# Optimization experiments

Measured on AMD Instinct MI355X. Metric: run time of the kernel, lower is better.

Reference implementation:

```python
import jax, jax.numpy as jnp
import numpy as np
import math

B, N, H, NH, HD, G = 2, 1024, 512, 8, 64, 50
MAX_DIST = 10.0


def setup_inputs() -> dict:
    key = jax.random.key(0)
    ks = jax.random.split(key, 12)
    s = 0.02  # small init scale for weights
    return {
        'x': jax.random.normal(ks[0], (B, N, H), jnp.float32),
        'distances': jax.random.uniform(ks[1], (B, N, N), jnp.float32) * MAX_DIST,
        'mask': jnp.ones((B, N), jnp.int32),
        'widths': jnp.ones((G,), jnp.float32) * 0.5,
        'dp_w': jax.random.normal(ks[2], (G, NH), jnp.float32) * s,
        'dp_b': jnp.zeros((NH,), jnp.float32),
        'wq': jax.random.normal(ks[3], (H, H), jnp.float32) * s,
        'bq': jnp.zeros((H,), jnp.float32),
        'wk': jax.random.normal(ks[4], (H, H), jnp.float32) * s,
        'bk': jnp.zeros((H,), jnp.float32),
        'wv': jax.random.normal(ks[5], (H, H), jnp.float32) * s,
        'bv': jnp.zeros((H,), jnp.float32),
        'wo': jax.random.normal(ks[6], (H, H), jnp.float32) * s,
        'bo': jnp.zeros((H,), jnp.float32),
        'ln1_g': jnp.ones((H,), jnp.float32),
        'ln1_b': jnp.zeros((H,), jnp.float32),
        'ln2_g': jnp.ones((H,), jnp.float32),
        'ln2_b': jnp.zeros((H,), jnp.float32),
        'w1': jax.random.normal(ks[7], (H, 4 * H), jnp.float32) * s,
        'b1': jnp.zeros((4 * H,), jnp.float32),
        'w2': jax.random.normal(ks[8], (4 * H, H), jnp.float32) * s,
        'b2': jnp.zeros((H,), jnp.float32),
    }


def _layernorm(x, g, b, eps=1e-5):
    mu = jnp.mean(x, axis=-1, keepdims=True)
    var = jnp.mean(jnp.square(x - mu), axis=-1, keepdims=True)
    return (x - mu) * jax.lax.rsqrt(var + eps) * g + b


def reference(x, distances, mask, widths, dp_w, dp_b, wq, bq, wk, bk, wv, bv,
              wo, bo, ln1_g, ln1_b, ln2_g, ln2_b, w1, b1, w2, b2):
    centers = jnp.linspace(0.0, MAX_DIST, G, dtype=jnp.float32)  # buffer

    residual = x
    xn = _layernorm(x, ln1_g, ln1_b)

    def split_heads(t):  # [B,N,H] -> [B,NH,N,HD]
        return t.reshape(B, N, NH, HD).transpose(0, 2, 1, 3)

    q = split_heads(xn @ wq + bq)
    k = split_heads(xn @ wk + bk)
    v = split_heads(xn @ wv + bv)

    scores = jnp.einsum('bhqd,bhkd->bhqk', q, k) / math.sqrt(HD)

    # Gaussian distance encoding: [B,N,N,G]
    diff = distances[..., None] - centers
    gf = jnp.exp(-jnp.square(diff) / (2.0 * jnp.square(widths)))
    # project to per-head bias, then permute to [B,NH,N,N]
    dist_bias = (gf @ dp_w + dp_b).transpose(0, 3, 1, 2)
    scores = scores + dist_bias

    key_mask = mask[:, None, None, :]  # [B,1,1,N]
    scores = jnp.where(key_mask == 0, -1e9, scores)

    attn = jax.nn.softmax(scores, axis=-1)
    out = jnp.einsum('bhqk,bhkd->bhqd', attn, v)
    out = out.transpose(0, 2, 1, 3).reshape(B, N, H)
    out = out @ wo + bo

    x = residual + out
    residual = x
    xn = _layernorm(x, ln2_g, ln2_b)
    h = jax.nn.gelu(xn @ w1 + b1, approximate=False)  # dropout is identity in eval
    x = residual + (h @ w2 + b2)
    return x
```

## Files before the change

kernel.cpp:

```cpp
#include <hip/hip_runtime.h>
#include <hip/hip_bf16.h>
#include <math.h>

#define B_ 2
#define N_ 1024
#define H_ 512
#define NH_ 8
#define HD_ 64
#define G_ 50
#define TAB_ 1024
constexpr float MAXD = 10.0f;

typedef __attribute__((ext_vector_type(8))) short short8;
typedef __attribute__((ext_vector_type(4))) float f32x4;

__device__ inline ushort f2bf(float v) {
  __hip_bfloat16 h = __float2bfloat16(v);
  return *(ushort*)&h;
}
__device__ inline float bf2f(ushort u) {
  unsigned x = ((unsigned)u) << 16;
  return __uint_as_float(x);
}
__device__ inline void gload_lds16(const ushort* g, ushort* l) {
  __builtin_amdgcn_global_load_lds(
      (const __attribute__((address_space(1))) void*)g,
      (__attribute__((address_space(3))) void*)l, 16, 0, 0);
}

__device__ inline void transp_dev(const float* __restrict__ src,
                                  ushort* __restrict__ d, int R, int C,
                                  int bx, int by, int t, float (*tile)[33]) {
  int r0 = by * 32, c0 = bx * 32;
  int rr = t >> 5, cc = t & 31;
  #pragma unroll
  for (int p = 0; p < 4; ++p)
    tile[rr + p * 8][cc] = src[(size_t)(r0 + rr + p * 8) * C + c0 + cc];
  __syncthreads();
  #pragma unroll
  for (int p = 0; p < 4; ++p)
    d[(size_t)(c0 + rr + p * 8) * R + r0 + cc] = f2bf(tile[cc][rr + p * 8]);
}

__global__ __launch_bounds__(256) void prep_k(
    const float* wq, const float* wk, const float* wv, const float* wo,
    const float* w1, const float* w2, ushort* __restrict__ wT4,
    ushort* __restrict__ w1T, ushort* __restrict__ w2T,
    const float* __restrict__ widths, const float* __restrict__ dp_w,
    const float* __restrict__ dp_b, float2* __restrict__ tab2,
    const float* __restrict__ x, const float* __restrict__ ln1g,
    const float* __restrict__ ln1b, ushort* __restrict__ xn) {
  __shared__ float tile[32][33];
  __shared__ float red2[4][2];
  int bid = blockIdx.x, t = threadIdx.x;
  if (bid < 1024) {
    int z = bid >> 8, rem = bid & 255;
    const float* src = (z == 0) ? wq : (z == 1) ? wk : (z == 2) ? wv : wo;
    transp_dev(src, wT4 + (size_t)z * 512 * 512, 512, 512, rem & 15, rem >> 4, t, tile);
  } else if (bid < 2048) {
    int rem = bid - 1024;
    transp_dev(w1, w1T, 512, 2048, rem & 63, rem >> 6, t, tile);
  } else if (bid < 3072) {
    int rem = bid - 2048;
    transp_dev(w2, w2T, 2048, 512, rem & 15, rem >> 4, t, tile);
  } else if (bid < 3105) {
    int i = (bid - 3072) * 256 + t;
    if (i >= NH_ * (TAB_ + 1)) return;
    int h = i / (TAB_ + 1), tt = i % (TAB_ + 1);
    int t1 = tt < TAB_ ? tt + 1 : tt;
    float d0 = (float)tt * (MAXD / TAB_);
    float d1 = (float)t1 * (MAXD / TAB_);
    float v0 = dp_b[h], v1 = dp_b[h];
    for (int g = 0; g < G_; ++g) {
      float c = (float)g * (MAXD / 49.0f);
      float w = widths[g];
      float inv = -1.0f / (2.0f * w * w);
      float wg = dp_w[g * NH_ + h];
      float e0 = d0 - c, e1 = d1 - c;
      v0 += expf(e0 * e0 * inv) * wg;
      v1 += expf(e1 * e1 * inv) * wg;
    }
    tab2[i] = make_float2(v0, v1);
  } else {
    int row = (bid - 3105) * 2 + (t >> 7);
    int tl = t & 127;
    float4 v = *(const float4*)(x + (size_t)row * H_ + tl * 4);
    float s = v.x + v.y + v.z + v.w;
    float sq = v.x * v.x + v.y * v.y + v.z * v.z + v.w * v.w;
    #pragma unroll
    for (int m = 1; m < 64; m <<= 1) {
      s += __shfl_xor(s, m, 64);
      sq += __shfl_xor(sq, m, 64);
    }
    int wid = t >> 6;
    if ((t & 63) == 0) { red2[wid][0] = s; red2[wid][1] = sq; }
    __syncthreads();
    int rw = (t >> 7) * 2;
    s = red2[rw][0] + red2[rw + 1][0];
    sq = red2[rw][1] + red2[rw + 1][1];
    float mu = s * (1.0f / H_);
    float var = sq * (1.0f / H_) - mu * mu;
    float rs = rsqrtf(var + 1e-5f);
    float4 gg = *(const float4*)(ln1g + tl * 4);
    float4 bb = *(const float4*)(ln1b + tl * 4);
    ushort4 o;
    o.x = f2bf((v.x - mu) * rs * gg.x + bb.x);
    o.y = f2bf((v.y - mu) * rs * gg.y + bb.y);
    o.z = f2bf((v.z - mu) * rs * gg.z + bb.z);
    o.w = f2bf((v.w - mu) * rs * gg.w + bb.w);
    *(ushort4*)(xn + (size_t)row * H_ + tl * 4) = o;
  }
}

enum { EPI_QKV = 1, EPI_RES = 2, EPI_GELU = 3, EPI_PART = 4 };

template <int BM, int BN, int EPI>
__global__ __launch_bounds__(256) void mfma_gemm(const ushort* __restrict__ A,
                                                 const ushort* __restrict__ Bt,
                                                 const float* __restrict__ b0,
                                                 const float* __restrict__ b1,
                                                 const float* __restrict__ b2,
                                                 const float* __restrict__ resid,
                                                 void* __restrict__ outv,
                                                 int K, int Ks, int Nc) {
  __shared__ ushort As[2][BM * 32];
  __shared__ ushort Bs[2][BN * 32];
  int t = threadIdx.x;
  int z = blockIdx.z;
  const ushort* Bz = Bt + (size_t)z * Nc * Ks;
  const float* bias = (z == 0) ? b0 : (z == 1) ? b1 : b2;
  int m0 = blockIdx.y * BM, n0 = blockIdx.x * BN;
  int lane = t & 63, w = t >> 6, wr = w >> 1, wc = w & 1;
  int lrow = lane & 15, lkg = lane >> 4;
  constexpr int NFM = BM / 32, NFN = BN / 32;
  constexpr int AL = BM / 64, BL = BN / 64;
  f32x4 acc[NFM][NFN] = {};
  int rl = lane >> 2, kgl = lane & 3;

  auto stage = [&](int buf, int kt) {
    #pragma unroll
    for (int p = 0; p < AL; ++p) {
      int r = w * (BM / 4) + p * 16 + rl;
      int kgs = kgl ^ (r & 3);
      gload_lds16(&A[(size_t)(m0 + r) * Ks + kt + kgs * 8],
                  &As[buf][(w * (BM / 4) + p * 16) * 32]);
    }
    #pragma unroll
    for (int p = 0; p < BL; ++p) {
      int r = w * (BN / 4) + p * 16 + rl;
      int kgs = kgl ^ (r & 3);
      gload_lds16(&Bz[(size_t)(n0 + r) * Ks + kt + kgs * 8],
                  &Bs[buf][(w * (BN / 4) + p * 16) * 32]);
    }
  };
  auto compute = [&](int buf) {
    short8 af[NFM], bfr[NFN];
    #pragma unroll
    for (int fm = 0; fm < NFM; ++fm) {
      int r = wr * (BM / 2) + fm * 16 + lrow;
      af[fm] = *(const short8*)&As[buf][r * 32 + ((lkg ^ (r & 3)) << 3)];
    }
    #pragma unroll
    for (int fn = 0; fn < NFN; ++fn) {
      int r = wc * (BN / 2) + fn * 16 + lrow;
      bfr[fn] = *(const short8*)&Bs[buf][r * 32 + ((lkg ^ (r & 3)) << 3)];
    }
    #pragma unroll
    for (int fm = 0; fm < NFM; ++fm)
      #pragma unroll
      for (int fn = 0; fn < NFN; ++fn)
        acc[fm][fn] = __builtin_amdgcn_mfma_f32_16x16x32_bf16(af[fm], bfr[fn],
                                                              acc[fm][fn], 0, 0, 0);
  };

  stage(0, 0);
  __syncthreads();
  int cur = 0;
  for (int kt = 0; kt < K; kt += 32) {
    if (kt + 32 < K) stage(cur ^ 1, kt + 32);
    compute(cur);
    __syncthreads();
    cur ^= 1;
  }

  int rbase = (lane >> 4) * 4;
  if constexpr (EPI == EPI_QKV) {
    if (z < 2) {
      #pragma unroll
      for (int fm = 0; fm < NFM; ++fm)
        #pragma unroll
        for (int fn = 0; fn < NFN; ++fn)
          #pragma unroll
          for (int j = 0; j < 4; ++j) {
            int row = m0 + wr * (BM / 2) + fm * 16 + rbase + j;
            int col = n0 + wc * (BN / 2) + fn * 16 + lrow;
            float v = acc[fm][fn][j] + bias[col];
            ushort* q = (ushort*)outv + (size_t)z * (1 << 20);
            int bb = row >> 10, n = row & (N_ - 1);
            int h = col >> 6, d = col & 63;
            q[(((size_t)(bb * NH_ + h)) * N_ + n) * HD_ + d] = f2bf(v);
          }
    } else {
      __shared__ float vtile[64 * 65];
      #pragma unroll
      for (int fm = 0; fm < NFM; ++fm)
        #pragma unroll
        for (int fn = 0; fn < NFN; ++fn)
          #pragma unroll
          for (int j = 0; j < 4; ++j) {
            int rloc = wr * (BM / 2) + fm * 16 + rbase + j;
            int cloc = wc * (BN / 2) + fn * 16 + lrow;
            vtile[rloc * 65 + cloc] = acc[fm][fn][j] + bias[n0 + cloc];
          }
      __syncthreads();
      int d_ = t & 63, nc = t >> 6;
      int h = n0 >> 6;
      int bb = m0 >> 10, nbase = m0 & (N_ - 1);
      ushort* dst = (ushort*)outv + (size_t)2 * (1 << 20) +
                    (((size_t)(bb * NH_ + h)) * HD_ + d_) * N_ + nbase + nc * 16;
      short8 o0, o1;
      #pragma unroll
      for (int i = 0; i < 8; ++i) {
        o0[i] = (short)f2bf(vtile[(nc * 16 + i) * 65 + d_]);
        o1[i] = (short)f2bf(vtile[(nc * 16 + 8 + i) * 65 + d_]);
      }
      *(short8*)&dst[0] = o0;
      *(short8*)&dst[8] = o1;
    }
  } else {
    #pragma unroll
    for (int fm = 0; fm < NFM; ++fm) {
      #pragma unroll
      for (int fn = 0; fn < NFN; ++fn) {
        #pragma unroll
        for (int j = 0; j < 4; ++j) {
          int row = m0 + wr * (BM / 2) + fm * 16 + rbase + j;
          int col = n0 + wc * (BN / 2) + fn * 16 + lrow;
          float v = acc[fm][fn][j] + bias[col];
          if constexpr (EPI == EPI_RES) {
            ((float*)outv)[(size_t)row * Nc + col] =
                resid[(size_t)row * Nc + col] + v;
          } else {
            ((ushort*)outv)[(size_t)row * Nc + col] =
                f2bf(0.5f * v * (1.0f + erff(v * 0.70710678118654752f)));
          }
        }
      }
    }
  }
}

template <int EPI>
__global__ __launch_bounds__(512) void mfma_gemm2(const ushort* __restrict__ A,
                                                  const ushort* __restrict__ Bt,
                                                  const float* __restrict__ bias,
                                                  const float* __restrict__ resid,
                                                  void* __restrict__ outv,
                                                  int K, int Ks, int Nc) {
  constexpr int BM = 64, BN = 64;
  __shared__ ushort AsBs[2][2][2][BM * 32];
  int t = threadIdx.x;
  int half = t >> 8;
  int lane = t & 63;
  int wl = (t >> 6) & 3;
  int wr = wl >> 1, wc = wl & 1;
  int lrow = lane & 15, lkg = lane >> 4;
  int k0 = half * K;
  int m0 = blockIdx.y * BM, n0 = blockIdx.x * BN;
  f32x4 acc[2][2] = {};
  int rl = lane >> 2, kgl = lane & 3;

  auto stage = [&](int buf, int kt) {
    int r = wl * 16 + rl;
    int kgs = kgl ^ (r & 3);
    gload_lds16(&A[(size_t)(m0 + r) * Ks + k0 + kt + kgs * 8],
                &AsBs[0][half][buf][(wl * 16) * 32]);
    gload_lds16(&Bt[(size_t)(n0 + r) * Ks + k0 + kt + kgs * 8],
                &AsBs[1][half][buf][(wl * 16) * 32]);
  };
  auto compute = [&](int buf) {
    short8 af[2], bfr[2];
    #pragma unroll
    for (int fm = 0; fm < 2; ++fm) {
      int r = wr * 32 + fm * 16 + lrow;
      af[fm] = *(const short8*)&AsBs[0][half][buf][r * 32 + ((lkg ^ (r & 3)) << 3)];
    }
    #pragma unroll
    for (int fn = 0; fn < 2; ++fn) {
      int r = wc * 32 + fn * 16 + lrow;
      bfr[fn] = *(const short8*)&AsBs[1][half][buf][r * 32 + ((lkg ^ (r & 3)) << 3)];
    }
    #pragma unroll
    for (int fm = 0; fm < 2; ++fm)
      #pragma unroll
      for (int fn = 0; fn < 2; ++fn)
        acc[fm][fn] = __builtin_amdgcn_mfma_f32_16x16x32_bf16(af[fm], bfr[fn],
                                                              acc[fm][fn], 0, 0, 0);
  };

  stage(0, 0);
  __syncthreads();
  int cur = 0;
  for (int kt = 0; kt < K; kt += 32) {
    if (kt + 32 < K) stage(cur ^ 1, kt + 32);
    compute(cur);
    __syncthreads();
    cur ^= 1;
  }

  float* red = (float*)&AsBs[0][0][0][0];
  int rbase = (lane >> 4) * 4;
  if (half == 1) {
    #pragma unroll
    for (int fm = 0; fm < 2; ++fm)
      #pragma unroll
      for (int fn = 0; fn < 2; ++fn)
        #pragma unroll
        for (int j = 0; j < 4; ++j) {
          int rloc = wr * 32 + fm * 16 + rbase + j;
          int cloc = wc * 32 + fn * 16 + lrow;
          red[rloc * 65 + cloc] = acc[fm][fn][j];
        }
  }
  __syncthreads();
  if (half == 0) {
    #pragma unroll
    for (int fm = 0; fm < 2; ++fm)
      #pragma unroll
      for (int fn = 0; fn < 2; ++fn)
        #pragma unroll
        for (int j = 0; j < 4; ++j) {
          int rloc = wr * 32 + fm * 16 + rbase + j;
          int cloc = wc * 32 + fn * 16 + lrow;
          float sum = acc[fm][fn][j] + red[rloc * 65 + cloc];
          int row = m0 + rloc, col = n0 + cloc;
          if constexpr (EPI == EPI_PART) {
            ((float*)outv)[(size_t)row * Nc + col] = sum;
          } else {
            ((float*)outv)[(size_t)row * Nc + col] =
                resid[(size_t)row * Nc + col] + sum + bias[col];
          }
        }
  }
}

__global__ __launch_bounds__(128) void comb2ln_k(const float* __restrict__ p,
                                                 const float* __restrict__ resid,
                                                 const float* __restrict__ bias,
                                                 const float* __restrict__ g,
                                                 const float* __restrict__ bl,
                                                 float* __restrict__ x1out,
                                                 ushort* __restrict__ xnout) {
  int row = blockIdx.x, t = threadIdx.x;
  int base = row * H_ + t * 4;
  f32x4 a = *(const f32x4*)&p[base];
  f32x4 r = *(const f32x4*)&resid[base];
  f32x4 bi = *(const f32x4*)&bias[t * 4];
  f32x4 v = r + a + bi;
  *(f32x4*)&x1out[base] = v;
  float s = v[0] + v[1] + v[2] + v[3];
  float sq = v[0] * v[0] + v[1] * v[1] + v[2] * v[2] + v[3] * v[3];
  #pragma unroll
  for (int m = 1; m < 64; m <<= 1) {
    s += __shfl_xor(s, m, 64);
    sq += __shfl_xor(sq, m, 64);
  }
  __shared__ float red[2][2];
  int wid = t >> 6;
  if ((t & 63) == 0) { red[wid][0] = s; red[wid][1] = sq; }
  __syncthreads();
  s = red[0][0] + red[1][0];
  sq = red[0][1] + red[1][1];
  float mu = s * (1.0f / H_);
  float var = sq * (1.0f / H_) - mu * mu;
  float rs = rsqrtf(var + 1e-5f);
  float4 gg = *(const float4*)(g + t * 4);
  float4 bb = *(const float4*)(bl + t * 4);
  ushort4 o;
  o.x = f2bf((v[0] - mu) * rs * gg.x + bb.x);
  o.y = f2bf((v[1] - mu) * rs * gg.y + bb.y);
  o.z = f2bf((v[2] - mu) * rs * gg.z + bb.z);
  o.w = f2bf((v[3] - mu) * rs * gg.w + bb.w);
  *(ushort4*)(xnout + (size_t)row * H_ + t * 4) = o;
}

constexpr int QT = 64, KT = 64, NJH = 2, NTH = N_ / (KT * NJH);
constexpr int JH = N_ / NJH;

__global__ __launch_bounds__(256) void attn_k(
    const ushort* __restrict__ q, const ushort* __restrict__ k,
    const ushort* __restrict__ v, const float* __restrict__ dist,
    const int* __restrict__ mask, const float2* __restrict__ tab2g,
    float* __restrict__ Op, float2* __restrict__ ml) {
  int qt = blockIdx.x, h = blockIdx.y, z = blockIdx.z;
  int b = z >> 1, jh = z & 1;
  int i0 = qt * QT;
  int jbase = jh * JH;
  __shared__ ushort Ks[2][KT * 64];
  __shared__ ushort Vt[2][64 * KT];
  __shared__ ushort Ps[4][16 * 64];
  __shared__ float2 tl2[TAB_ + 1];
  __shared__ float mfl[JH];
  int t = threadIdx.x;
  int lane = t & 63, w = t >> 6;
  int l = lane & 15, g = lane >> 4;

  for (int i = t; i <= TAB_; i += 256) tl2[i] = tab2g[h * (TAB_ + 1) + i];
  for (int i = t; i < JH; i += 256) mfl[i] = (mask[b * N_ + jbase + i] == 0) ? -1e9f : 0.0f;

  const size_t ho = ((size_t)(b * NH_ + h)) * N_ * HD_;
  const ushort* qb = q + ho;
  const ushort* kb = k + ho;
  const ushort* vb = v + ho;

  int qloc = w * 16 + 4 * g;
  int qrow = i0 + w * 16 + l;
  short8 qf[2];
  qf[0] = *(const short8*)&qb[(size_t)qrow * 64 + g * 8];
  qf[1] = *(const short8*)&qb[(size_t)qrow * 64 + 32 + g * 8];

  int c2 = t & 7, jr = t >> 3;

  auto stK = [&](int buf, short8 val, int j2) {
    *(short8*)&Ks[buf][j2 * 64 + ((c2 ^ (j2 & 7)) << 3)] = val;
  };
  auto stV = [&](int buf, short8 val, int d) {
    *(short8*)&Vt[buf][d * 64 + ((c2 ^ (d & 7)) << 3)] = val;
  };

  const float* dbase = dist + ((size_t)b * N_ + (i0 + qloc)) * N_ + jbase + l;

  short8 k0a, k1a, v0a, v1a;
  float ddc[4][4], ddn[4][4];
  {
    const ushort* kn = kb + (size_t)jbase * 64;
    const ushort* vn = vb + jbase;
    k0a = *(const short8*)&kn[(size_t)jr * 64 + c2 * 8];
    k1a = *(const short8*)&kn[(size_t)(jr + 32) * 64 + c2 * 8];
    v0a = *(const short8*)&vn[(size_t)jr * N_ + c2 * 8];
    v1a = *(const short8*)&vn[(size_t)(jr + 32) * N_ + c2 * 8];
    #pragma unroll
    for (int reg = 0; reg < 4; ++reg)
      #pragma unroll
      for (int fj = 0; fj < 4; ++fj)
        ddc[reg][fj] = dbase[(size_t)reg * N_ + fj * 16];
  }
  __syncthreads();
  stK(0, k0a, jr); stK(0, k1a, jr + 32);
  stV(0, v0a, jr); stV(0, v1a, jr + 32);
  __syncthreads();

  float m_[4] = {-1e30f, -1e30f, -1e30f, -1e30f};
  float l_[4] = {0.f, 0.f, 0.f, 0.f};
  f32x4 acc[4] = {{0,0,0,0},{0,0,0,0},{0,0,0,0},{0,0,0,0}};

  int cur = 0;
  for (int tt = 0; tt < NTH; ++tt) {
    const int j0 = jbase + tt * KT;
    if (tt + 1 < NTH) {
      const ushort* kn = kb + (size_t)(j0 + KT) * 64;
      const ushort* vn = vb + (j0 + KT);
      k0a = *(const short8*)&kn[(size_t)jr * 64 + c2 * 8];
      k1a = *(const short8*)&kn[(size_t)(jr + 32) * 64 + c2 * 8];
      v0a = *(const short8*)&vn[(size_t)jr * N_ + c2 * 8];
      v1a = *(const short8*)&vn[(size_t)(jr + 32) * N_ + c2 * 8];
      #pragma unroll
      for (int reg = 0; reg < 4; ++reg)
        #pragma unroll
        for (int fj = 0; fj < 4; ++fj)
          ddn[reg][fj] = dbase[(size_t)reg * N_ + (tt + 1) * KT + fj * 16];
    }
    f32x4 sa[4] = {{0,0,0,0},{0,0,0,0},{0,0,0,0},{0,0,0,0}};
    __builtin_amdgcn_s_setprio(1);
    #pragma unroll
    for (int dblk = 0; dblk < 2; ++dblk)
      #pragma unroll
      for (int fj = 0; fj < 4; ++fj) {
        int j2 = fj * 16 + l;
        short8 kf = *(const short8*)&Ks[cur][j2 * 64 + (((dblk * 4 + g) ^ (j2 & 7)) << 3)];
        sa[fj] = __builtin_amdgcn_mfma_f32_16x16x32_bf16(qf[dblk], kf, sa[fj], 0, 0, 0);
      }
    __builtin_amdgcn_s_setprio(0);
    float al_[4];
    #pragma unroll
    for (int reg = 0; reg < 4; ++reg) {
      float svr[4];
      #pragma unroll
      for (int fj = 0; fj < 4; ++fj) {
        float u = ddc[reg][fj] * ((float)TAB_ / MAXD);
        int it = (int)u;
        it = it < 0 ? 0 : (it > TAB_ - 1 ? TAB_ - 1 : it);
        float f = u - (float)it;
        float2 tv = tl2[it];
        float bias = tv.x + f * (tv.y - tv.x) + mfl[tt * KT + fj * 16 + l];
        svr[fj] = fmaf(sa[fj][reg], 0.125f, bias);
      }
      float rm = fmaxf(fmaxf(svr[0], svr[1]), fmaxf(svr[2], svr[3]));
      rm = fmaxf(rm, __shfl_xor(rm, 1, 64));
      rm = fmaxf(rm, __shfl_xor(rm, 2, 64));
      rm = fmaxf(rm, __shfl_xor(rm, 4, 64));
      rm = fmaxf(rm, __shfl_xor(rm, 8, 64));
      float mn = fmaxf(m_[reg], rm);
      float al = __expf(m_[reg] - mn);
      m_[reg] = mn;
      al_[reg] = al;
      float ps = 0.f;
      int qlq = 4 * g + reg;
      #pragma unroll
      for (int fj = 0; fj < 4; ++fj) {
        float p = __expf(svr[fj] - mn);
        ps += p;
        int c = fj * 2 + (l >> 3);
        Ps[w][qlq * 64 + ((c ^ (qlq & 7)) << 3) + (l & 7)] = f2bf(p);
      }
      ps += __shfl_xor(ps, 1, 64);
      ps += __shfl_xor(ps, 2, 64);
      ps += __shfl_xor(ps, 4, 64);
      ps += __shfl_xor(ps, 8, 64);
      l_[reg] = l_[reg] * al + ps;
    }
    #pragma unroll
    for (int fd = 0; fd < 4; ++fd)
      #pragma unroll
      for (int reg = 0; reg < 4; ++reg) acc[fd][reg] *= al_[reg];
    __builtin_amdgcn_s_setprio(1);
    #pragma unroll
    for (int jj = 0; jj < 2; ++jj) {
      short8 pa = *(const short8*)&Ps[w][l * 64 + (((jj * 4 + g) ^ (l & 7)) << 3)];
      #pragma unroll
      for (int fd = 0; fd < 4; ++fd) {
        int d2 = fd * 16 + l;
        short8 vf = *(const short8*)&Vt[cur][d2 * 64 + (((jj * 4 + g) ^ (d2 & 7)) << 3)];
        acc[fd] = __builtin_amdgcn_mfma_f32_16x16x32_bf16(pa, vf, acc[fd], 0, 0, 0);
      }
    }
    __builtin_amdgcn_s_setprio(0);
    if (tt + 1 < NTH) {
      int nb = cur ^ 1;
      stK(nb, k0a, jr); stK(nb, k1a, jr + 32);
      stV(nb, v0a, jr); stV(nb, v1a, jr + 32);
      #pragma unroll
      for (int reg = 0; reg < 4; ++reg)
        #pragma unroll
        for (int fj = 0; fj < 4; ++fj) ddc[reg][fj] = ddn[reg][fj];
    }
    __syncthreads();
    cur ^= 1;
  }
  const size_t pbase = (((size_t)(b * NJH + jh) * NH_ + h) * N_) + i0;
  #pragma unroll
  for (int reg = 0; reg < 4; ++reg) {
    int rowl = w * 16 + 4 * g + reg;
    float* op = Op + (pbase + rowl) * HD_ + l;
    #pragma unroll
    for (int fd = 0; fd < 4; ++fd) op[fd * 16] = acc[fd][reg];
    if (l == 0) ml[pbase + rowl] = make_float2(m_[reg], l_[reg]);
  }
}

__global__ __launch_bounds__(256) void comb_k(const float* __restrict__ Op,
                                              const float2* __restrict__ ml,
                                              ushort* __restrict__ ao) {
  int idx = blockIdx.x * 256 + threadIdx.x;
  int row = idx >> 4;
  int dq = (idx & 15) * 4;
  int b = row >> 13, h = (row >> 10) & 7, n = row & 1023;
  size_t p0 = (((size_t)(b * NJH + 0) * NH_ + h) * N_) + n;
  size_t p1 = (((size_t)(b * NJH + 1) * NH_ + h) * N_) + n;
  float2 v0 = ml[p0], v1 = ml[p1];
  float M = fmaxf(v0.x, v1.x);
  float a0 = __expf(v0.x - M), a1 = __expf(v1.x - M);
  float inv = 1.0f / (v0.y * a0 + v1.y * a1);
  float4 O0 = *(const float4*)&Op[p0 * HD_ + dq];
  float4 O1 = *(const float4*)&Op[p1 * HD_ + dq];
  ushort4 o;
  o.x = f2bf((O0.x * a0 + O1.x * a1) * inv);
  o.y = f2bf((O0.y * a0 + O1.y * a1) * inv);
  o.z = f2bf((O0.z * a0 + O1.z * a1) * inv);
  o.w = f2bf((O0.w * a0 + O1.w * a1) * inv);
  *(ushort4*)&ao[((size_t)(b * N_ + n)) * H_ + h * HD_ + dq] = o;
}

extern "C" void kernel_launch(void* const* d_in, const int* in_sizes, int n_in,
                              void* d_out, int out_size, void* d_ws, size_t ws_size,
                              hipStream_t stream) {
  const float* x = (const float*)d_in[0];
  const float* distances = (const float*)d_in[1];
  const int* mask = (const int*)d_in[2];
  const float* widths = (const float*)d_in[3];
  const float* dp_w = (const float*)d_in[4];
  const float* dp_b = (const float*)d_in[5];
  const float* wq = (const float*)d_in[6];
  const float* bq = (const float*)d_in[7];
  const float* wk = (const float*)d_in[8];
  const float* bk = (const float*)d_in[9];
  const float* wv = (const float*)d_in[10];
  const float* bv = (const float*)d_in[11];
  const float* wo = (const float*)d_in[12];
  const float* bo = (const float*)d_in[13];
  const float* ln1_g = (const float*)d_in[14];
  const float* ln1_b = (const float*)d_in[15];
  const float* ln2_g = (const float*)d_in[16];
  const float* ln2_b = (const float*)d_in[17];
  const float* w1 = (const float*)d_in[18];
  const float* b1 = (const float*)d_in[19];
  const float* w2 = (const float*)d_in[20];
  const float* b2 = (const float*)d_in[21];
  float* out = (float*)d_out;
  float* wsf = (float*)d_ws;

  const size_t M1 = (size_t)1 << 20;
  ushort* qkvb = (ushort*)wsf;
  float* x1 = wsf + 2 * M1;
  ushort* hbuf = (ushort*)(wsf + 3 * M1);
  ushort* xn = (ushort*)(wsf + 5 * M1);
  ushort* xn2 = (ushort*)(wsf + 5 * M1 + M1 / 2);
  ushort* ao = (ushort*)(wsf + 6 * M1);
  ushort* wT4 = (ushort*)(wsf + 6 * M1 + M1 / 2);
  ushort* w1T = (ushort*)(wsf + 7 * M1);
  ushort* w2T = (ushort*)(wsf + 7 * M1 + M1 / 2);
  float2* tab2 = (float2*)(wsf + 8 * M1);
  float* Op = wsf + 9 * M1;
  float2* ml = (float2*)(wsf + 11 * M1);
  float* pAO = wsf + 12 * M1;

  prep_k<<<4129, 256, 0, stream>>>(wq, wk, wv, wo, w1, w2, wT4, w1T, w2T,
                                   widths, dp_w, dp_b, tab2, x, ln1_g, ln1_b, xn);

  mfma_gemm<64, 64, EPI_QKV><<<dim3(8, 32, 3), 256, 0, stream>>>(
      xn, wT4, bq, bk, bv, nullptr, qkvb, 512, 512, 512);

  attn_k<<<dim3(N_ / QT, NH_, B_ * NJH), 256, 0, stream>>>(
      qkvb, qkvb + M1, qkvb + 2 * M1, distances, mask, tab2, Op, ml);
  comb_k<<<1024, 256, 0, stream>>>(Op, ml, ao);

  mfma_gemm2<EPI_PART><<<dim3(8, 32), 512, 0, stream>>>(
      ao, wT4 + (size_t)3 * 512 * 512, bo, nullptr, pAO, 256, 512, 512);
  comb2ln_k<<<B_ * N_, 128, 0, stream>>>(pAO, x, bo, ln2_g, ln2_b, x1, xn2);

  mfma_gemm<128, 64, EPI_GELU><<<dim3(32, 16, 1), 256, 0, stream>>>(
      xn2, w1T, b1, b1, b1, nullptr, hbuf, 512, 512, 2048);

  mfma_gemm2<EPI_RES><<<dim3(8, 32), 512, 0, stream>>>(
      hbuf, w2T, b2, x1, out, 1024, 2048, 512);
}
```

Baseline: 98.81 us.

## Fuse split-KV combine into attention kernel via last-arriver atomic flag

Removes the separate comb_k launch. Each attention block writes its partial output and softmax stats, bumps a per-tile atomic counter, and the second block to finish merges both halves and writes the bf16 output through LDS. This saves a kernel launch and a full reread pass over the partial buffers. In exchange it adds a memset, threadfences and an atomic, and the last block still has to read the other half's partials.

```diff
diff --git a/kernel.cpp b/kernel.cpp
--- a/kernel.cpp
+++ b/kernel.cpp
@@ -391,7 +391,8 @@
     const ushort* __restrict__ q, const ushort* __restrict__ k,
     const ushort* __restrict__ v, const float* __restrict__ dist,
     const int* __restrict__ mask, const float2* __restrict__ tab2g,
-    float* __restrict__ Op, float2* __restrict__ ml) {
+    float* __restrict__ Op, float2* __restrict__ ml,
+    unsigned* __restrict__ flags, ushort* __restrict__ aout) {
   int qt = blockIdx.x, h = blockIdx.y, z = blockIdx.z;
   int b = z >> 1, jh = z & 1;
   int i0 = qt * QT;
@@ -401,6 +402,7 @@
   __shared__ ushort Ps[4][16 * 64];
   __shared__ float2 tl2[TAB_ + 1];
   __shared__ float mfl[JH];
+  __shared__ int lastflag;
   int t = threadIdx.x;
   int lane = t & 63, w = t >> 6;
   int l = lane & 15, g = lane >> 4;
@@ -550,35 +552,44 @@
   const size_t pbase = (((size_t)(b * NJH + jh) * NH_ + h) * N_) + i0;
   #pragma unroll
   for (int reg = 0; reg < 4; ++reg) {
-    int rowl = w * 16 + 4 * g + reg;
+    int rowl = qloc + reg;
     float* op = Op + (pbase + rowl) * HD_ + l;
     #pragma unroll
     for (int fd = 0; fd < 4; ++fd) op[fd * 16] = acc[fd][reg];
     if (l == 0) ml[pbase + rowl] = make_float2(m_[reg], l_[reg]);
   }
-}
-
-__global__ __launch_bounds__(256) void comb_k(const float* __restrict__ Op,
-                                              const float2* __restrict__ ml,
-                                              ushort* __restrict__ ao) {
-  int idx = blockIdx.x * 256 + threadIdx.x;
-  int row = idx >> 4;
-  int dq = (idx & 15) * 4;
-  int b = row >> 13, h = (row >> 10) & 7, n = row & 1023;
-  size_t p0 = (((size_t)(b * NJH + 0) * NH_ + h) * N_) + n;
-  size_t p1 = (((size_t)(b * NJH + 1) * NH_ + h) * N_) + n;
-  float2 v0 = ml[p0], v1 = ml[p1];
-  float M = fmaxf(v0.x, v1.x);
-  float a0 = __expf(v0.x - M), a1 = __expf(v1.x - M);
-  float inv = 1.0f / (v0.y * a0 + v1.y * a1);
-  float4 O0 = *(const float4*)&Op[p0 * HD_ + dq];
-  float4 O1 = *(const float4*)&Op[p1 * HD_ + dq];
-  ushort4 o;
-  o.x = f2bf((O0.x * a0 + O1.x * a1) * inv);
-  o.y = f2bf((O0.y * a0 + O1.y * a1) * inv);
-  o.z = f2bf((O0.z * a0 + O1.z * a1) * inv);
-  o.w = f2bf((O0.w * a0 + O1.w * a1) * inv);
-  *(ushort4*)&ao[((size_t)(b * N_ + n)) * H_ + h * HD_ + dq] = o;
+  __threadfence();
+  __syncthreads();
+  if (t == 0) {
+    unsigned old = atomicAdd(&flags[((unsigned)(b * NH_ + h)) * (N_ / QT) + qt], 1u);
+    lastflag = (old == 1) ? 1 : 0;
+  }
+  __syncthreads();
+  if (!lastflag) return;
+  __threadfence();
+  ushort* otile = (ushort*)&Ks[0][0];
+  const size_t pother = (((size_t)(b * NJH + (jh ^ 1)) * NH_ + h) * N_) + i0;
+  #pragma unroll
+  for (int reg = 0; reg < 4; ++reg) {
+    int rowl = qloc + reg;
+    float2 mo = ml[pother + rowl];
+    float M = fmaxf(m_[reg], mo.x);
+    float aw = __expf(m_[reg] - M), ax = __expf(mo.x - M);
+    float inv = 1.0f / (l_[reg] * aw + mo.y * ax);
+    #pragma unroll
+    for (int fd = 0; fd < 4; ++fd) {
+      float oo = Op[(pother + rowl) * HD_ + fd * 16 + l];
+      otile[rowl * 68 + fd * 16 + l] =
+          f2bf((acc[fd][reg] * aw + oo * ax) * inv);
+    }
+  }
+  __syncthreads();
+  {
+    int r = t >> 2, seg = t & 3;
+    ushort* dst = aout + ((size_t)(b * N_ + i0 + r)) * H_ + h * HD_ + seg * 16;
+    *(short8*)&dst[0] = *(const short8*)&otile[r * 68 + seg * 16];
+    *(short8*)&dst[8] = *(const short8*)&otile[r * 68 + seg * 16 + 8];
+  }
 }
 
 extern "C" void kernel_launch(void* const* d_in, const int* in_sizes, int n_in,
@@ -623,6 +634,9 @@
   float* Op = wsf + 9 * M1;
   float2* ml = (float2*)(wsf + 11 * M1);
   float* pAO = wsf + 12 * M1;
+  unsigned* flags = (unsigned*)(wsf + 13 * M1);
+
+  hipMemsetAsync(flags, 0, 256 * sizeof(unsigned), stream);
 
   prep_k<<<4129, 256, 0, stream>>>(wq, wk, wv, wo, w1, w2, wT4, w1T, w2T,
                                    widths, dp_w, dp_b, tab2, x, ln1_g, ln1_b, xn);
@@ -631,8 +645,7 @@
       xn, wT4, bq, bk, bv, nullptr, qkvb, 512, 512, 512);
 
   attn_k<<<dim3(N_ / QT, NH_, B_ * NJH), 256, 0, stream>>>(
-      qkvb, qkvb + M1, qkvb + 2 * M1, distances, mask, tab2, Op, ml);
-  comb_k<<<1024, 256, 0, stream>>>(Op, ml, ao);
+      qkvb, qkvb + M1, qkvb + 2 * M1, distances, mask, tab2, Op, ml, flags, ao);
 
   mfma_gemm2<EPI_PART><<<dim3(8, 32), 512, 0, stream>>>(
       ao, wT4 + (size_t)3 * 512 * 512, bo, nullptr, pAO, 256, 512, 512);
```

Measured after the change: 180.5 us. 1.83x slower.
